# Kernel tuning notes

Measured on AMD Instinct MI355X. Metric: run time of the kernel, lower is better.

Reference implementation:

```python
import jax, jax.numpy as jnp
import numpy as np

B, T, D = 2, 2048, 1024
H, KVH, HD = 16, 4, 64  # query heads, kv heads, head_dim
GROUPS = H // KVH


def apply_rope(x, cos, sin):
    # x: (B, nh, T, hd); cos/sin: (max_T, hd//2)
    t = x.shape[2]
    c = cos[:t][None, None]  # (1,1,T,hd//2)
    s = sin[:t][None, None]
    half = x.shape[-1] // 2
    x1, x2 = x[..., :half], x[..., half:]
    rotated = jnp.concatenate((-x2, x1), axis=-1)
    cf = jnp.concatenate((c, c), axis=-1)  # repeat(1,1,1,2)
    sf = jnp.concatenate((s, s), axis=-1)
    return x * cf + rotated * sf


def setup_inputs():
    key = jax.random.key(0)
    ks = jax.random.split(key, 5)
    x = jax.random.normal(ks[0], (B, T, D), dtype=jnp.float32)
    # RoPE tables: theta^(-i/half) frequencies
    half = HD // 2
    inv_freq = 1.0 / (10000.0 ** (jnp.arange(half, dtype=jnp.float32) / half))
    ang = jnp.arange(T, dtype=jnp.float32)[:, None] * inv_freq[None, :]  # (T, half)
    rope_cos = jnp.cos(ang)
    rope_sin = jnp.sin(ang)
    # Causal additive mask
    causal = jnp.tril(jnp.ones((T, T), dtype=bool))
    attention_mask = jnp.where(causal, 0.0, -1e9).astype(jnp.float32)[None, None]
    scale = 0.02
    Wq = jax.random.normal(ks[1], (D, D), dtype=jnp.float32) * scale
    Wk = jax.random.normal(ks[2], (D, KVH * HD), dtype=jnp.float32) * scale
    Wv = jax.random.normal(ks[3], (D, KVH * HD), dtype=jnp.float32) * scale
    Wo = jax.random.normal(ks[4], (D, D), dtype=jnp.float32) * scale
    return {"x": x, "rope_cos": rope_cos, "rope_sin": rope_sin,
            "attention_mask": attention_mask,
            "Wq": Wq, "Wk": Wk, "Wv": Wv, "Wo": Wo}


def reference(x, rope_cos, rope_sin, attention_mask, Wq, Wk, Wv, Wo):
    b, t, _ = x.shape
    q = (x @ Wq).reshape(b, t, H, HD).transpose(0, 2, 1, 3)      # (B,H,T,hd)
    k = (x @ Wk).reshape(b, t, KVH, HD).transpose(0, 2, 1, 3)    # (B,KVH,T,hd)
    v = (x @ Wv).reshape(b, t, KVH, HD).transpose(0, 2, 1, 3)
    q = apply_rope(q, rope_cos, rope_sin)
    k = apply_rope(k, rope_cos, rope_sin)
    if GROUPS > 1:
        k = jnp.repeat(k, GROUPS, axis=1)  # repeat_interleave over heads
        v = jnp.repeat(v, GROUPS, axis=1)
    scale = 1.0 / np.sqrt(HD)
    attn = jnp.einsum('bhqd,bhkd->bhqk', q, k) * scale
    attn = attn + attention_mask
    attn = jax.nn.softmax(attn.astype(jnp.float32), axis=-1).astype(q.dtype)
    out = jnp.einsum('bhqk,bhkd->bhqd', attn, v)
    out = out.transpose(0, 2, 1, 3).reshape(b, t, D)
    return out @ Wo
```

## Files before the change

kernel.cpp:

```cpp
#include <hip/hip_runtime.h>

typedef __attribute__((ext_vector_type(8))) short short8;
typedef __attribute__((ext_vector_type(4))) short short4v;
typedef __attribute__((ext_vector_type(4))) float f32x4;

#define T_ 2048
#define H_ 16
#define KVH_ 4
#define QSCALE 0.18033688011112042f
#define DEFER 8.0f

__device__ inline unsigned short f2bf(float f) {
    unsigned u = __builtin_bit_cast(unsigned, f);
    u += 0x7fff + ((u >> 16) & 1);
    return (unsigned short)(u >> 16);
}

__device__ inline void gl_lds16(const unsigned short* g, unsigned short* lds) {
    __builtin_amdgcn_global_load_lds(
        (const __attribute__((address_space(1))) unsigned int*)g,
        (__attribute__((address_space(3))) unsigned int*)lds, 16, 0, 0);
}

__global__ void cast_bf16(const float* __restrict__ in,
                          unsigned short* __restrict__ out, int n8) {
    int i = blockIdx.x * blockDim.x + threadIdx.x;
    if (i >= n8) return;
    float4 v0 = ((const float4*)in)[i * 2];
    float4 v1 = ((const float4*)in)[i * 2 + 1];
    short8 o;
    o[0] = f2bf(v0.x); o[1] = f2bf(v0.y); o[2] = f2bf(v0.z); o[3] = f2bf(v0.w);
    o[4] = f2bf(v1.x); o[5] = f2bf(v1.y); o[6] = f2bf(v1.z); o[7] = f2bf(v1.w);
    ((short8*)out)[i] = o;
}

__global__ __launch_bounds__(256) void transpose_cast(
        const float* __restrict__ W, unsigned short* __restrict__ out,
        int K, int N, int rowoff) {
    __shared__ unsigned short ts[64][66];
    const int bx = blockIdx.x, by = blockIdx.y, tid = threadIdx.x;
    #pragma unroll
    for (int s = 0; s < 16; ++s) {
        int idx = tid + s * 256;
        int kl = idx >> 6, nl = idx & 63;
        ts[kl][nl] = f2bf(W[(size_t)(by * 64 + kl) * N + bx * 64 + nl]);
    }
    __syncthreads();
    #pragma unroll
    for (int s = 0; s < 16; ++s) {
        int idx = tid + s * 256;
        int nl = idx >> 6, kl = idx & 63;
        out[(size_t)(rowoff + bx * 64 + nl) * K + by * 64 + kl] = ts[kl][nl];
    }
}

template <int MODE>
__global__ __launch_bounds__(256) void gemm_mfma(
        const unsigned short* __restrict__ A,
        const unsigned short* __restrict__ Bt,
        void* __restrict__ Cq, unsigned short* __restrict__ Ck,
        unsigned short* __restrict__ Cvt,
        const float* __restrict__ rc, const float* __restrict__ rs,
        int M, int N, int K) {
    __shared__ __align__(16) unsigned short As[128 * 32];
    __shared__ __align__(16) unsigned short Bs[64 * 32];
    const int tid = threadIdx.x;
    const int w = tid >> 6, l = tid & 63, lk = l & 15, lg = l >> 4;
    const int bx = blockIdx.x, by = blockIdx.y;

    const unsigned short* Arow = A + (size_t)by * 128 * K;
    const unsigned short* Brow = Bt + (size_t)bx * 64 * K;

    f32x4 acc[2][4];
    #pragma unroll
    for (int m = 0; m < 2; ++m)
        #pragma unroll
        for (int n = 0; n < 4; ++n) acc[m][n] = (f32x4){0, 0, 0, 0};

    for (int k0 = 0; k0 < K; k0 += 32) {
        #pragma unroll
        for (int p = 0; p < 2; ++p) {
            int cb = p * 256 + w * 64;
            int c = cb + l;
            int row = c >> 2, ko = (c & 3) * 8;
            gl_lds16(Arow + (size_t)row * K + k0 + ko, As + cb * 8);
        }
        {
            int c = w * 64 + l;
            int row = c >> 2, ko = (c & 3) * 8;
            gl_lds16(Brow + (size_t)row * K + k0 + ko, Bs + c * 8);
        }
        __syncthreads();
        short8 aF[2], bF[4];
        #pragma unroll
        for (int m = 0; m < 2; ++m)
            aF[m] = *(const short8*)&As[(w * 32 + m * 16 + lk) * 32 + lg * 8];
        #pragma unroll
        for (int n = 0; n < 4; ++n)
            bF[n] = *(const short8*)&Bs[(n * 16 + lk) * 32 + lg * 8];
        #pragma unroll
        for (int m = 0; m < 2; ++m)
            #pragma unroll
            for (int n = 0; n < 4; ++n)
                acc[m][n] = __builtin_amdgcn_mfma_f32_16x16x32_bf16(
                    aF[m], bF[n], acc[m][n], 0, 0, 0);
        __syncthreads();
    }

    const int rowbase = by * 128 + w * 32;
    if constexpr (MODE == 0) {
        float* C = (float*)Cq;
        #pragma unroll
        for (int m = 0; m < 2; ++m)
            #pragma unroll
            for (int r = 0; r < 4; ++r) {
                size_t ro = (size_t)(rowbase + m * 16 + lg * 4 + r) * N + bx * 64 + lk;
                #pragma unroll
                for (int n = 0; n < 4; ++n) C[ro + n * 16] = acc[m][n][r];
            }
    }
    if constexpr (MODE == 1) {
        const int colgrp = bx;
        if (colgrp < 16) {
            unsigned short* C = (unsigned short*)Cq;
            const int h = colgrp;
            #pragma unroll
            for (int m = 0; m < 2; ++m)
                #pragma unroll
                for (int r = 0; r < 4; ++r) {
                    int trow = rowbase + m * 16 + lg * 4 + r;
                    int b = trow >> 11, t = trow & (T_ - 1);
                    size_t ob = (((size_t)(b * 16 + h)) * T_ + t) * 64;
                    #pragma unroll
                    for (int n = 0; n < 2; ++n) {
                        int d = n * 16 + lk;
                        float cc = rc[t * 32 + d], ss = rs[t * 32 + d];
                        float x1 = acc[m][n][r], x2 = acc[m][n + 2][r];
                        C[ob + d]      = f2bf((x1 * cc - x2 * ss) * QSCALE);
                        C[ob + d + 32] = f2bf((x2 * cc + x1 * ss) * QSCALE);
                    }
                }
        } else if (colgrp < 20) {
            const int kvh = colgrp - 16;
            #pragma unroll
            for (int m = 0; m < 2; ++m)
                #pragma unroll
                for (int r = 0; r < 4; ++r) {
                    int trow = rowbase + m * 16 + lg * 4 + r;
                    int b = trow >> 11, t = trow & (T_ - 1);
                    size_t ob = (((size_t)(b * 4 + kvh)) * T_ + t) * 64;
                    #pragma unroll
                    for (int n = 0; n < 2; ++n) {
                        int d = n * 16 + lk;
                        float cc = rc[t * 32 + d], ss = rs[t * 32 + d];
                        float x1 = acc[m][n][r], x2 = acc[m][n + 2][r];
                        Ck[ob + d]      = f2bf(x1 * cc - x2 * ss);
                        Ck[ob + d + 32] = f2bf(x2 * cc + x1 * ss);
                    }
                }
        } else {
            const int kvh = colgrp - 20;
            #pragma unroll
            for (int m = 0; m < 2; ++m) {
                int trow0 = rowbase + m * 16 + lg * 4;
                int b = trow0 >> 11, t0 = trow0 & (T_ - 1);
                #pragma unroll
                for (int n = 0; n < 4; ++n) {
                    int d = n * 16 + lk;
                    short4v pk;
                    #pragma unroll
                    for (int r = 0; r < 4; ++r) pk[r] = f2bf(acc[m][n][r]);
                    *(short4v*)(Cvt + (((size_t)(b * 4 + kvh)) * 64 + d) * T_ + t0) = pk;
                }
            }
        }
    }
}

#define SW(row, col) ((col) ^ (((row) & 7) << 3))

__global__ __launch_bounds__(256) void attn_mfma(
        const unsigned short* __restrict__ Q,
        const unsigned short* __restrict__ K,
        const unsigned short* __restrict__ Vt,
        unsigned short* __restrict__ O) {
    __shared__ __align__(16) unsigned short Ks[2][64][64];
    __shared__ __align__(16) unsigned short Vs[2][64][64];
    __shared__ __align__(16) unsigned short Pl[4][16][64];

    const int bid = blockIdx.x;
    const int bh = bid & 31;
    const int u  = bid >> 5;
    const int g = u >> 3, k = u & 7;
    const int qt = (g == 0) ? k : (g == 1) ? 15 - k : (g == 2) ? 16 + k : 31 - k;
    const int h = bh & 15;
    const int b = bh >> 4;
    const int kv = h >> 2;
    const int tid = threadIdx.x;
    const int w = tid >> 6, l = tid & 63;
    const int lk = l & 15, lg = l >> 4;

    const unsigned short* Kb = K + ((size_t)(b * 4 + kv)) * T_ * 64;
    const unsigned short* Vb = Vt + ((size_t)(b * 4 + kv)) * 64 * T_;

    short8 af0, af1;
    {
        const unsigned short* q0 =
            Q + (((size_t)(b * 16 + h)) * T_ + qt * 64 + w * 16 + lk) * 64 + lg * 8;
        af0 = *(const short8*)(q0);
        af1 = *(const short8*)(q0 + 32);
    }

    f32x4 acc[4];
    f32x4 lacc = {0, 0, 0, 0};
    float mrow[4];
    #pragma unroll
    for (int db = 0; db < 4; ++db) acc[db] = (f32x4){0, 0, 0, 0};
    #pragma unroll
    for (int r = 0; r < 4; ++r) mrow[r] = -1e38f;

    short8 ones;
    #pragma unroll
    for (int i = 0; i < 8; ++i) ones[i] = (short)0x3F80;

    const int srow = tid >> 2;
    const int soff = (tid & 3) * 16;

    short8 kr0, kr1, vr0, vr1;
    auto load_kv = [&](int kt) {
        const unsigned short* kg = Kb + ((size_t)(kt * 64 + srow)) * 64 + soff;
        kr0 = *(const short8*)(kg);
        kr1 = *(const short8*)(kg + 8);
        const unsigned short* vg = Vb + (size_t)srow * T_ + kt * 64 + soff;
        vr0 = *(const short8*)(vg);
        vr1 = *(const short8*)(vg + 8);
    };
    auto write_kv = [&](int buf) {
        *(short8*)(&Ks[buf][srow][SW(srow, soff)])     = kr0;
        *(short8*)(&Ks[buf][srow][SW(srow, soff + 8)]) = kr1;
        *(short8*)(&Vs[buf][srow][SW(srow, soff)])     = vr0;
        *(short8*)(&Vs[buf][srow][SW(srow, soff + 8)]) = vr1;
    };

    for (int kt = 0; kt <= qt; ++kt) {
        const int cur = kt & 1;
        if (kt == 0) { load_kv(0); write_kv(0); }
        __syncthreads();
        const bool pf = kt < qt;
        if (pf) load_kv(kt + 1);

        float s4[4][4];
        __builtin_amdgcn_s_setprio(1);
        #pragma unroll
        for (int nt = 0; nt < 4; ++nt) {
            const int row = nt * 16 + lk;
            short8 b0 = *(const short8*)(&Ks[cur][row][SW(row, lg * 8)]);
            short8 b1 = *(const short8*)(&Ks[cur][row][SW(row, 32 + lg * 8)]);
            f32x4 c = {0, 0, 0, 0};
            c = __builtin_amdgcn_mfma_f32_16x16x32_bf16(af0, b0, c, 0, 0, 0);
            c = __builtin_amdgcn_mfma_f32_16x16x32_bf16(af1, b1, c, 0, 0, 0);
            #pragma unroll
            for (int r = 0; r < 4; ++r) s4[nt][r] = c[r];
        }
        __builtin_amdgcn_s_setprio(0);

        if (kt == qt) {
            int qloc = w * 16 + lg * 4;
            #pragma unroll
            for (int nt = 0; nt < 4; ++nt) {
                int kloc = nt * 16 + lk;
                #pragma unroll
                for (int r = 0; r < 4; ++r)
                    if (kloc > qloc + r) s4[nt][r] = -1e30f;
            }
        }

        float rm[4];
        #pragma unroll
        for (int r = 0; r < 4; ++r) {
            float v = fmaxf(fmaxf(s4[0][r], s4[1][r]), fmaxf(s4[2][r], s4[3][r]));
            v = fmaxf(v, __shfl_xor(v, 1));
            v = fmaxf(v, __shfl_xor(v, 2));
            v = fmaxf(v, __shfl_xor(v, 4));
            v = fmaxf(v, __shfl_xor(v, 8));
            rm[r] = v;
        }
        bool need = (rm[0] > mrow[0] + DEFER) || (rm[1] > mrow[1] + DEFER) ||
                    (rm[2] > mrow[2] + DEFER) || (rm[3] > mrow[3] + DEFER);
        if (__any(need)) {
            #pragma unroll
            for (int r = 0; r < 4; ++r) {
                float nm = fmaxf(mrow[r], rm[r]);
                float corr = exp2f(mrow[r] - nm);
                mrow[r] = nm;
                #pragma unroll
                for (int db = 0; db < 4; ++db) acc[db][r] *= corr;
                lacc[r] *= corr;
            }
        }
        #pragma unroll
        for (int r = 0; r < 4; ++r)
            #pragma unroll
            for (int nt = 0; nt < 4; ++nt) s4[nt][r] = exp2f(s4[nt][r] - mrow[r]);

        #pragma unroll
        for (int nt = 0; nt < 4; ++nt)
            #pragma unroll
            for (int r = 0; r < 4; ++r) {
                int row = lg * 4 + r;
                Pl[w][row][SW(row, nt * 16 + lk)] = f2bf(s4[nt][r]);
            }

        if (pf) write_kv(cur ^ 1);

        __builtin_amdgcn_s_setprio(1);
        #pragma unroll
        for (int kk = 0; kk < 2; ++kk) {
            short8 pa = *(const short8*)(&Pl[w][lk][SW(lk, kk * 32 + lg * 8)]);
            lacc = __builtin_amdgcn_mfma_f32_16x16x32_bf16(pa, ones, lacc, 0, 0, 0);
            #pragma unroll
            for (int db = 0; db < 4; ++db) {
                const int row = db * 16 + lk;
                short8 vb = *(const short8*)(&Vs[cur][row][SW(row, kk * 32 + lg * 8)]);
                acc[db] = __builtin_amdgcn_mfma_f32_16x16x32_bf16(pa, vb, acc[db], 0, 0, 0);
            }
        }
        __builtin_amdgcn_s_setprio(0);
    }

    #pragma unroll
    for (int r = 0; r < 4; ++r) {
        float inv = 1.f / lacc[r];
        int t = qt * 64 + w * 16 + lg * 4 + r;
        #pragma unroll
        for (int db = 0; db < 4; ++db)
            O[(((size_t)(b * T_ + t)) * 16 + h) * 64 + db * 16 + lk] =
                f2bf(acc[db][r] * inv);
    }
}

extern "C" void kernel_launch(void* const* d_in, const int* in_sizes, int n_in,
                              void* d_out, int out_size, void* d_ws, size_t ws_size,
                              hipStream_t stream) {
    const float* x  = (const float*)d_in[0];
    const float* rc = (const float*)d_in[1];
    const float* rs = (const float*)d_in[2];
    const float* Wq = (const float*)d_in[4];
    const float* Wk = (const float*)d_in[5];
    const float* Wv = (const float*)d_in[6];
    const float* Wo = (const float*)d_in[7];
    float* out = (float*)d_out;

    unsigned short* ws = (unsigned short*)d_ws;
    unsigned short* xb  = ws;
    unsigned short* Wt  = ws + 4194304;
    unsigned short* Wot = ws + 5767168;
    unsigned short* Qbf = ws + 6815744;
    unsigned short* Kbf = ws + 11010048;
    unsigned short* Vtb = ws + 12058624;
    unsigned short* Ob  = ws + 13107200;

    dim3 blk(256);
    cast_bf16<<<2048, blk, 0, stream>>>(x, xb, 524288);
    transpose_cast<<<dim3(16, 16), blk, 0, stream>>>(Wq, Wt, 1024, 1024, 0);
    transpose_cast<<<dim3(4, 16),  blk, 0, stream>>>(Wk, Wt, 1024, 256, 1024);
    transpose_cast<<<dim3(4, 16),  blk, 0, stream>>>(Wv, Wt, 1024, 256, 1280);
    transpose_cast<<<dim3(16, 16), blk, 0, stream>>>(Wo, Wot, 1024, 1024, 0);

    gemm_mfma<1><<<dim3(24, 32), blk, 0, stream>>>(
        xb, Wt, (void*)Qbf, Kbf, Vtb, rc, rs, 4096, 1536, 1024);

    attn_mfma<<<dim3(1024), blk, 0, stream>>>(Qbf, Kbf, Vtb, Ob);

    gemm_mfma<0><<<dim3(16, 32), blk, 0, stream>>>(
        Ob, Wot, (void*)out, nullptr, nullptr, nullptr, nullptr, 4096, 1024, 1024);
}
```

Before: 129.8 us.

## Split long causal attention rows into two KV chunks with a combine kernel

```diff
diff --git a/kernel.cpp b/kernel.cpp
--- a/kernel.cpp
+++ b/kernel.cpp
@@ -14,6 +14,10 @@
     unsigned u = __builtin_bit_cast(unsigned, f);
     u += 0x7fff + ((u >> 16) & 1);
     return (unsigned short)(u >> 16);
+}
+__device__ inline float bf2f(unsigned short v) {
+    unsigned u = ((unsigned)v) << 16;
+    return __builtin_bit_cast(float, u);
 }
 
 __device__ inline void gl_lds16(const unsigned short* g, unsigned short* lds) {
@@ -183,16 +187,28 @@
         const unsigned short* __restrict__ Q,
         const unsigned short* __restrict__ K,
         const unsigned short* __restrict__ Vt,
-        unsigned short* __restrict__ O) {
+        unsigned short* __restrict__ O,
+        float* __restrict__ PM, float* __restrict__ PLp,
+        unsigned short* __restrict__ PACC) {
     __shared__ __align__(16) unsigned short Ks[2][64][64];
     __shared__ __align__(16) unsigned short Vs[2][64][64];
     __shared__ __align__(16) unsigned short Pl[4][16][64];
 
     const int bid = blockIdx.x;
-    const int bh = bid & 31;
-    const int u  = bid >> 5;
-    const int g = u >> 3, k = u & 7;
-    const int qt = (g == 0) ? k : (g == 1) ? 15 - k : (g == 2) ? 16 + k : 31 - k;
+    int bh, qt, kt0, nkt, ck;
+    bool direct;
+    if (bid < 512) {
+        bh = bid & 31; qt = 16 + ((bid >> 5) & 15);
+        kt0 = 0; nkt = 16; ck = 0; direct = false;
+    } else if (bid < 1024) {
+        int j = bid - 512;
+        bh = j & 31; qt = 15 - ((j >> 5) & 15);
+        kt0 = 0; nkt = qt + 1; ck = 0; direct = true;
+    } else {
+        int j = bid - 1024;
+        bh = j & 31; qt = 31 - ((j >> 5) & 15);
+        kt0 = 16; nkt = qt - 15; ck = 1; direct = false;
+    }
     const int h = bh & 15;
     const int b = bh >> 4;
     const int kv = h >> 2;
@@ -242,11 +258,13 @@
         *(short8*)(&Vs[buf][srow][SW(srow, soff + 8)]) = vr1;
     };
 
-    for (int kt = 0; kt <= qt; ++kt) {
-        const int cur = kt & 1;
-        if (kt == 0) { load_kv(0); write_kv(0); }
+    load_kv(kt0);
+    write_kv(0);
+    for (int i = 0; i < nkt; ++i) {
+        const int kt = kt0 + i;
+        const int cur = i & 1;
         __syncthreads();
-        const bool pf = kt < qt;
+        const bool pf = i < nkt - 1;
         if (pf) load_kv(kt + 1);
 
         float s4[4][4];
@@ -328,15 +346,64 @@
         __builtin_amdgcn_s_setprio(0);
     }
 
-    #pragma unroll
-    for (int r = 0; r < 4; ++r) {
-        float inv = 1.f / lacc[r];
-        int t = qt * 64 + w * 16 + lg * 4 + r;
-        #pragma unroll
-        for (int db = 0; db < 4; ++db)
-            O[(((size_t)(b * T_ + t)) * 16 + h) * 64 + db * 16 + lk] =
-                f2bf(acc[db][r] * inv);
-    }
+    if (direct) {
+        #pragma unroll
+        for (int r = 0; r < 4; ++r) {
+            float inv = 1.f / lacc[r];
+            int t = qt * 64 + w * 16 + lg * 4 + r;
+            #pragma unroll
+            for (int db = 0; db < 4; ++db)
+                O[(((size_t)(b * T_ + t)) * 16 + h) * 64 + db * 16 + lk] =
+                    f2bf(acc[db][r] * inv);
+        }
+    } else {
+        const int p = ((bh << 4) + (qt - 16)) * 2 + ck;
+        #pragma unroll
+        for (int r = 0; r < 4; ++r) {
+            int row = w * 16 + lg * 4 + r;
+            if (lk == 0) {
+                PM[p * 64 + row]  = mrow[r];
+                PLp[p * 64 + row] = lacc[r];
+            }
+            #pragma unroll
+            for (int db = 0; db < 4; ++db)
+                PACC[((size_t)p * 64 + row) * 64 + db * 16 + lk] = f2bf(acc[db][r]);
+        }
+    }
+}
+
+__global__ __launch_bounds__(256) void combine_attn(
+        const float* __restrict__ PM, const float* __restrict__ PLp,
+        const unsigned short* __restrict__ PACC,
+        unsigned short* __restrict__ O) {
+    const int cid = blockIdx.x;
+    const int bh = cid & 31, qt = 16 + (cid >> 5);
+    const int h = bh & 15, b = bh >> 4;
+    const int tid = threadIdx.x;
+    const int rr = tid >> 2, cg = (tid & 3) * 16;
+    const int p0 = ((bh << 4) + (qt - 16)) * 2, p1 = p0 + 1;
+
+    float mA = PM[p0 * 64 + rr], mB = PM[p1 * 64 + rr];
+    float lA = PLp[p0 * 64 + rr], lB = PLp[p1 * 64 + rr];
+    float M = fmaxf(mA, mB);
+    float wA = exp2f(mA - M), wB = exp2f(mB - M);
+    float inv = 1.f / (lA * wA + lB * wB);
+    wA *= inv; wB *= inv;
+
+    const unsigned short* a = &PACC[((size_t)p0 * 64 + rr) * 64 + cg];
+    const unsigned short* c = &PACC[((size_t)p1 * 64 + rr) * 64 + cg];
+    short8 va0 = *(const short8*)a, va1 = *(const short8*)(a + 8);
+    short8 vb0 = *(const short8*)c, vb1 = *(const short8*)(c + 8);
+    short8 o0, o1;
+    #pragma unroll
+    for (int i = 0; i < 8; ++i) {
+        o0[i] = f2bf(bf2f((unsigned short)va0[i]) * wA + bf2f((unsigned short)vb0[i]) * wB);
+        o1[i] = f2bf(bf2f((unsigned short)va1[i]) * wA + bf2f((unsigned short)vb1[i]) * wB);
+    }
+    int t = qt * 64 + rr;
+    unsigned short* op = &O[(((size_t)(b * T_ + t)) * 16 + h) * 64 + cg];
+    *(short8*)op = o0;
+    *(short8*)(op + 8) = o1;
 }
 
 extern "C" void kernel_launch(void* const* d_in, const int* in_sizes, int n_in,
@@ -360,6 +427,10 @@
     unsigned short* Vtb = ws + 12058624;
     unsigned short* Ob  = ws + 13107200;
 
+    float* PM          = (float*)d_ws;
+    float* PLp         = PM + 1024 * 64;
+    unsigned short* PACC = (unsigned short*)(PLp + 1024 * 64);
+
     dim3 blk(256);
     cast_bf16<<<2048, blk, 0, stream>>>(x, xb, 524288);
     transpose_cast<<<dim3(16, 16), blk, 0, stream>>>(Wq, Wt, 1024, 1024, 0);
@@ -370,7 +441,8 @@
     gemm_mfma<1><<<dim3(24, 32), blk, 0, stream>>>(
         xb, Wt, (void*)Qbf, Kbf, Vtb, rc, rs, 4096, 1536, 1024);
 
-    attn_mfma<<<dim3(1024), blk, 0, stream>>>(Qbf, Kbf, Vtb, Ob);
+    attn_mfma<<<dim3(1536), blk, 0, stream>>>(Qbf, Kbf, Vtb, Ob, PM, PLp, PACC);
+    combine_attn<<<dim3(512), blk, 0, stream>>>(PM, PLp, PACC, Ob);
 
     gemm_mfma<0><<<dim3(16, 32), blk, 0, stream>>>(
         Ob, Wot, (void*)out, nullptr, nullptr, nullptr, nullptr, 4096, 1024, 1024);
```

New measurement: 133.6 us. +2.9%, slower.
